# Kernel tuning notes

Hardware: AMD Instinct MI355X
Metric: run time of the kernel (lower is better)

Reference implementation:

```python
import jax, jax.numpy as jnp
import numpy as np

N, NB, NP, T = 1024, 16, 256, 80
EPS_LEN = 1e-9   # seg_len clamp_min in original
EPS_DD = 1e-12   # dot(d,d) clamp_min in original


def setup_inputs() -> dict:
    key = jax.random.key(0)
    k1, k2, k3, k4 = jax.random.split(key, 4)
    # smooth-ish random trajectory (cumsum of steps)
    selected_traj = jnp.cumsum(jax.random.normal(k1, (N, T, 3), jnp.float32) * 0.5, axis=1)
    # random polylines per (sample, boundary)
    road_points = jnp.cumsum(jax.random.normal(k2, (N, NB, NP, 3), jnp.float32) * 0.5, axis=2) \
                  + jax.random.normal(k3, (N, NB, 1, 3), jnp.float32) * 2.0
    # ragged valid-prefix masks, length in [2, NP]
    lengths = jax.random.randint(k4, (N, NB), 2, NP + 1)
    road_mask = jnp.arange(NP)[None, None, :] < lengths[:, :, None]
    return {"selected_traj": selected_traj, "road_points": road_points, "road_mask": road_mask}


def _arc_project(pos, rp, rm):
    # pos: [N,T,3]; rp: [N,NB,NP,3]; rm: [N,NB,NP] bool
    n, t = pos.shape[0], pos.shape[1]
    nb, npts = rp.shape[1], rp.shape[2]
    inf = jnp.asarray(jnp.inf, pos.dtype)
    ar = jnp.arange(npts)
    n_valid = rm.sum(-1)                                    # [N,NB]

    # pack valid points to the front, preserving order (== boolean-mask gather in torch)
    order = jnp.argsort(jnp.logical_not(rm), axis=-1, stable=True)
    pts_f = jnp.take_along_axis(rp, order[..., None], axis=2)      # [N,NB,NP,3]
    pack_mask = ar[None, None, :] < n_valid[:, :, None]
    pts_f = jnp.where(pack_mask[..., None], pts_f, 0.0)
    # flipped direction: reverse the valid prefix
    flip_idx = jnp.clip(n_valid[:, :, None] - 1 - ar[None, None, :], 0, npts - 1)
    pts_b = jnp.take_along_axis(pts_f, flip_idx[..., None], axis=2)
    pts_b = jnp.where(pack_mask[..., None], pts_b, 0.0)
    pts = jnp.stack([pts_f, pts_b], axis=2)                 # [N,NB,2,NP,3]

    # segment i is real iff i < n_valid-1
    seg_mask = ar[: npts - 1][None, None, None, :] < (n_valid - 1)[:, :, None, None]  # [N,NB,1,NP-1]
    seg_vec = pts[..., 1:, :] - pts[..., :-1, :]            # [N,NB,2,NP-1,3]
    seg_norm = jnp.sqrt((seg_vec ** 2).sum(-1))
    seg_len = jnp.where(seg_mask, jnp.maximum(seg_norm, EPS_LEN), 0.0)
    cum_s = jnp.concatenate([jnp.zeros_like(seg_len[..., :1]), jnp.cumsum(seg_len, -1)], -1)  # [N,NB,2,NP]
    last_idx = jnp.clip(n_valid - 1, 0, npts - 1)[:, :, None, None]
    total_s = jnp.take_along_axis(cum_s, jnp.broadcast_to(last_idx, (n, nb, 2, 1)), -1)  # [N,NB,2,1]

    # entry: project first trajectory point onto nearest valid segment
    p0 = pos[:, 0][:, None, None, None, :]                  # [N,1,1,1,3]
    a0 = pts[..., :-1, :]
    dd0 = jnp.maximum((seg_vec ** 2).sum(-1), EPS_DD)
    t0 = jnp.clip(((p0 - a0) * seg_vec).sum(-1) / dd0, 0.0, 1.0)
    q0 = a0 + t0[..., None] * seg_vec
    d2 = jnp.where(seg_mask, ((p0 - q0) ** 2).sum(-1), inf)
    seg0 = jnp.argmin(d2, -1)[..., None]                    # [N,NB,2,1]
    entry_s = jnp.take_along_axis(cum_s, seg0, -1) + jnp.take_along_axis(t0 * seg_len, seg0, -1)

    # trajectory arc-length, resample polyline at entry_s + traj arc length
    traj_seg = jnp.sqrt(((pos[:, 1:] - pos[:, :-1]) ** 2).sum(-1))
    traj_cs = jnp.concatenate([jnp.zeros_like(traj_seg[:, :1]), jnp.cumsum(traj_seg, -1)], -1)  # [N,T]
    target_s = jnp.clip(entry_s + traj_cs[:, None, None, :], 0.0, total_s)  # [N,NB,2,T]

    j = jax.vmap(lambda c, tg: jnp.searchsorted(c, tg, side='right'))(
        cum_s.reshape(-1, npts), target_s.reshape(-1, t)) - 1
    j = jnp.clip(j.reshape(n, nb, 2, t), 0, jnp.maximum(n_valid[:, :, None, None] - 2, 0))

    seg_l = jnp.take_along_axis(seg_len, j, -1)
    cs_j = jnp.take_along_axis(cum_s, j, -1)
    t_loc = jnp.clip((target_s - cs_j) / jnp.maximum(seg_l, EPS_LEN), 0.0, 1.0)
    pa = jnp.take_along_axis(pts, j[..., None], axis=3)
    pb = jnp.take_along_axis(pts, (j + 1)[..., None], axis=3)
    proj = pa + t_loc[..., None] * (pb - pa)                # [N,NB,2,T,3]

    # pick (boundary, direction) candidate with min total L2 cost
    cost = jnp.sqrt(((pos[:, None, None] - proj) ** 2).sum(-1)).sum(-1)  # [N,NB,2]
    cand_ok = (n_valid >= 2)[:, :, None]
    cost = jnp.where(cand_ok, cost, inf)
    best = jnp.argmin(cost.reshape(n, -1), -1)
    best_proj = jnp.take_along_axis(proj.reshape(n, -1, t, 3), best[:, None, None, None], axis=1)[:, 0]
    has = cand_ok.any((1, 2))
    return jnp.where(has[:, None, None], best_proj, pos)


def reference(selected_traj, road_points, road_mask):
    pos = selected_traj[..., 0:3]
    out_pos = _arc_project(pos, road_points, road_mask)
    return jnp.concatenate([out_pos, selected_traj[..., 3:]], axis=-1)
```

## Files before the change

kernel.cpp:

```cpp
#include <hip/hip_runtime.h>
#include <math.h>

#define NN 1024
#define NBB 16
#define NP 256
#define TT 80
#define EPS_LEN 1e-9f
#define EPS_DD 1e-12f

__device__ __forceinline__ float frcp(float x){ return __builtin_amdgcn_rcpf(x); }
__device__ __forceinline__ float fsq(float x){ return __builtin_amdgcn_sqrtf(x); }
__device__ __forceinline__ float rlane_f(float x, int l){
  return __builtin_bit_cast(float, __builtin_amdgcn_readlane(__builtin_bit_cast(int, x), l));
}
__device__ __forceinline__ float bump(float v){
  return __builtin_bit_cast(float, __builtin_bit_cast(int, v) + 1);
}

template<int CTRL,int RM>
__device__ __forceinline__ float dpp_add(float v){
  int t = __builtin_amdgcn_update_dpp(0, __builtin_bit_cast(int, v), CTRL, RM, 0xf, true);
  return v + __builtin_bit_cast(float, t);
}
__device__ __forceinline__ float wave_incl_scan(float v){
  v = dpp_add<0x111,0xf>(v);
  v = dpp_add<0x112,0xf>(v);
  v = dpp_add<0x114,0xf>(v);
  v = dpp_add<0x118,0xf>(v);
  v = dpp_add<0x142,0xa>(v);
  v = dpp_add<0x143,0xc>(v);
  return v;
}
__device__ __forceinline__ float wave_sum(float v){ return rlane_f(wave_incl_scan(v), 63); }
template<int CTRL,int RM>
__device__ __forceinline__ float dpp_min(float v){
  int t = __builtin_amdgcn_update_dpp(0x7f800000, __builtin_bit_cast(int,v), CTRL, RM, 0xf, false);
  return fminf(v, __builtin_bit_cast(float,t));
}
__device__ __forceinline__ float wave_min_all(float v){
  v=dpp_min<0x111,0xf>(v); v=dpp_min<0x112,0xf>(v);
  v=dpp_min<0x114,0xf>(v); v=dpp_min<0x118,0xf>(v);
  v=dpp_min<0x142,0xa>(v); v=dpp_min<0x143,0xc>(v);
  return rlane_f(v, 63);
}

__device__ __forceinline__ void lds_fence() {
  __builtin_amdgcn_wave_barrier();
  asm volatile("s_waitcnt lgkmcnt(0)" ::: "memory");
  __builtin_amdgcn_wave_barrier();
}

__device__ __forceinline__ int wave_nv(const void* mask, size_t base, int lane) {
  bool as_byte = ((const unsigned char*)mask)[1] != 0;
  int nv = 0;
  if (as_byte) {
    uchar4 v = ((const uchar4*)((const unsigned char*)mask + base))[lane];
    nv += __popcll(__ballot(v.x != 0));
    nv += __popcll(__ballot(v.y != 0));
    nv += __popcll(__ballot(v.z != 0));
    nv += __popcll(__ballot(v.w != 0));
  } else {
    int4 v = ((const int4*)((const int*)mask + base))[lane];
    nv += __popcll(__ballot(v.x != 0));
    nv += __popcll(__ballot(v.y != 0));
    nv += __popcll(__ballot(v.z != 0));
    nv += __popcll(__ballot(v.w != 0));
  }
  return nv;
}

__device__ __forceinline__ int count256s(const float* __restrict__ cs,
                                         const float* co, float v){
  int K = 0;
  #pragma unroll
  for (int k=0;k<16;k++) K += (co[k] < v);
  int base = (K < 16 ? K : 15) * 16;
  const float4* f4 = (const float4*)(cs + base);
  float4 c0=f4[0], c1=f4[1], c2=f4[2], c3=f4[3];
  int r = (c0.x<v)+(c0.y<v)+(c0.z<v)+(c0.w<v)+(c1.x<v)+(c1.y<v)+(c1.z<v)+(c1.w<v)
        + (c2.x<v)+(c2.y<v)+(c2.z<v)+(c2.w<v)+(c3.x<v)+(c3.y<v)+(c3.z<v)+(c3.w<v);
  return (K >= 16) ? 256 : (base + r);
}

struct SegOut {
  float cpre[4];
  float run;
  float bdf, btf; int bjf;
  float bdl, btl; int bjl;
};

template<bool NEEDMIN>
__device__ __forceinline__ void seg_pass(float4 A, float4 B, float4 C,
                                         int lane, int nv,
                                         float p0x, float p0y, float p0z,
                                         float* __restrict__ pts, SegOut& R) {
  const int j0 = lane * 4;
  float x[5], y[5], z[5];
  x[0]=A.x; y[0]=A.y; z[0]=A.z;
  x[1]=A.w; y[1]=B.x; z[1]=B.y;
  x[2]=B.z; y[2]=B.w; z[2]=C.x;
  x[3]=C.y; y[3]=C.z; z[3]=C.w;
  x[4]=__shfl_down(x[0],1,64); y[4]=__shfl_down(y[0],1,64); z[4]=__shfl_down(z[0],1,64);
  ((float4*)pts)[lane*3+0] = make_float4(x[0],y[0],z[0],x[1]);
  ((float4*)pts)[lane*3+1] = make_float4(y[1],z[1],x[2],y[2]);
  ((float4*)pts)[lane*3+2] = make_float4(z[2],x[3],y[3],z[3]);
  float run = 0.f;
  R.bdf=INFINITY; R.btf=0.f; R.bjf=j0;
  R.bdl=INFINITY; R.btl=0.f; R.bjl=j0;
  #pragma unroll
  for (int k=0;k<4;k++){
    bool valid = (j0+k) < nv-1;
    float vx=x[k+1]-x[k], vy=y[k+1]-y[k], vz=z[k+1]-z[k];
    float n2 = vx*vx+vy*vy+vz*vz;
    float sl = valid ? fmaxf(fsq(n2), EPS_LEN) : 0.f;
    if (NEEDMIN){
      float t = ((p0x-x[k])*vx+(p0y-y[k])*vy+(p0z-z[k])*vz) * frcp(fmaxf(n2,EPS_DD));
      t = fminf(fmaxf(t,0.f),1.f);
      float qx=x[k]+t*vx, qy=y[k]+t*vy, qz=z[k]+t*vz;
      float dx=p0x-qx, dy=p0y-qy, dz=p0z-qz;
      float d2 = valid ? (dx*dx+dy*dy+dz*dz) : INFINITY;
      if (d2 <  R.bdf){R.bdf=d2; R.bjf=j0+k; R.btf=t;}
      if (d2 <= R.bdl){R.bdl=d2; R.bjl=j0+k; R.btl=t;}
    }
    run += sl; R.cpre[k]=run;
  }
  R.run = run;
}

__device__ __forceinline__ void cs_pair_from_regs(int idx, float ex, const SegOut& R,
                                                  float& c0, float& c1){
  int o = idx >> 2, r = idx & 3;
  float a0 = (r==0)?0.f : (r==1)?R.cpre[0] : (r==2)?R.cpre[1] : R.cpre[2];
  float a1 = (r==0)?R.cpre[0] : (r==1)?R.cpre[1] : (r==2)?R.cpre[2] : R.run;
  c0 = rlane_f(ex + a0, idx >> 2);
  c1 = rlane_f(ex + a1, o);
}

__device__ __forceinline__ void interp_at(const float* __restrict__ pts,
                                          const float* __restrict__ cs,
                                          const float* co, float Tot, int nv, int jmaxv,
                                          int dir, float ts,
                                          float& prx, float& pry, float& prz){
  float vq = dir ? (Tot - ts) : bump(ts);
  int cnt = count256s(cs, co, vq);
  int j = dir ? (nv-1-cnt) : (cnt-1);
  j = j<0?0:(j>jmaxv?jmaxv:j);
  int ia = dir ? (nv-1-j) : j;
  int ib = dir ? (nv-2-j) : (j+1);
  int lo = dir ? ib : ia;
  float c_lo = cs[lo], c_hi = cs[lo+1];
  float base = dir ? (Tot - c_hi) : c_lo;
  float tl = (ts - base) * frcp(fmaxf(c_hi - c_lo, EPS_LEN));
  tl = fminf(fmaxf(tl,0.f),1.f);
  float3 PA = *(const float3*)(pts + ia*3);
  float3 PB = *(const float3*)(pts + ib*3);
  prx = PA.x + tl*(PB.x-PA.x);
  pry = PA.y + tl*(PB.y-PA.y);
  prz = PA.z + tl*(PB.z-PA.z);
}

__device__ __forceinline__ void traj_tcs_wave(const float* __restrict__ pos, int lane,
                                              float* __restrict__ s_tc,
                                              float3& ptl, float3& pB){
  ptl.x = pos[lane*3+0]; ptl.y = pos[lane*3+1]; ptl.z = pos[lane*3+2];
  pB = make_float3(0.f,0.f,0.f);
  if (lane < 16){
    int t = 64+lane;
    pB.x = pos[t*3+0]; pB.y = pos[t*3+1]; pB.z = pos[t*3+2];
  }
  float nx = __shfl_down(ptl.x,1,64), ny = __shfl_down(ptl.y,1,64), nz = __shfl_down(ptl.z,1,64);
  float bx0 = rlane_f(pB.x,0), by0 = rlane_f(pB.y,0), bz0 = rlane_f(pB.z,0);
  if (lane==63){ nx=bx0; ny=by0; nz=bz0; }
  float dx=nx-ptl.x, dy=ny-ptl.y, dz=nz-ptl.z;
  float segA = fsq(dx*dx+dy*dy+dz*dz);
  float mx = __shfl_down(pB.x,1,64), my = __shfl_down(pB.y,1,64), mz = __shfl_down(pB.z,1,64);
  float ex=mx-pB.x, ey=my-pB.y, ez=mz-pB.z;
  float segB = (lane<15) ? fsq(ex*ex+ey*ey+ez*ez) : 0.f;
  float incA = wave_incl_scan(segA);
  float totA = rlane_f(incA, 63);
  float incB = wave_incl_scan(segB);
  s_tc[lane+1] = incA;
  if (lane<15) s_tc[65+lane] = totA + incB;
  if (lane==0) s_tc[0] = 0.f;
}

__global__ __launch_bounds__(256, 8)
void cost_kernel(const float* __restrict__ traj, const float* __restrict__ rp,
                 const void* __restrict__ mask,
                 float* __restrict__ cost, float2* __restrict__ ent) {
  __shared__ float s_pts[4][NP*3], s_cs[4][NP], s_tc[4][TT];
  const int wid = threadIdx.x>>6, lane = threadIdx.x&63;
  const int nb = blockIdx.x*4 + wid;
  const int n = nb >> 4;
  const float* pos = traj + (size_t)n*TT*3;

  const float4* p4 = (const float4*)(rp + (size_t)nb*NP*3);
  float4 A = p4[lane*3+0], B = p4[lane*3+1], C = p4[lane*3+2];
  int nvr = wave_nv(mask, (size_t)nb*NP, lane);
  float3 ptl, pB;
  traj_tcs_wave(pos, lane, s_tc[wid], ptl, pB);

  if (nvr < 2){
    if (lane==0){ cost[nb*2+0]=INFINITY; cost[nb*2+1]=INFINITY; }
    return;
  }
  const int nv = nvr;
  float p0x = rlane_f(ptl.x,0), p0y = rlane_f(ptl.y,0), p0z = rlane_f(ptl.z,0);

  SegOut R;
  seg_pass<true>(A,B,C, lane, nv, p0x,p0y,p0z, s_pts[wid], R);

  float inc = wave_incl_scan(R.run);
  float ex = inc - R.run;
  ((float4*)s_cs[wid])[lane] = make_float4(ex, ex+R.cpre[0], ex+R.cpre[1], ex+R.cpre[2]);
  const float Tot = rlane_f(inc, 63);

  float cval = ex + R.cpre[2];
  float co[16];
  #pragma unroll
  for (int k=0;k<16;k++) co[k] = rlane_f(cval, 4*k+3);

  float minv = wave_min_all(R.bdf);
  unsigned long long mf = __ballot(R.bdf == minv);
  unsigned long long ml = __ballot(R.bdl == minv);
  int lf = __builtin_ctzll(mf);
  int ll = 63 - __builtin_clzll(ml);
  int   jf = __builtin_amdgcn_readlane(R.bjf, lf);
  float tf = rlane_f(R.btf, lf);
  int   jl = __builtin_amdgcn_readlane(R.bjl, ll);
  float tl0 = rlane_f(R.btl, ll);
  float cjf, cjf1, cjl, cjl1;
  cs_pair_from_regs(jf, ex, R, cjf, cjf1);
  cs_pair_from_regs(jl, ex, R, cjl, cjl1);
  float e0 = cjf + tf*(cjf1-cjf);
  float e1 = (Tot - cjl1) + (1.f-tl0)*(cjl1-cjl);

  lds_fence();

  const float* cs = s_cs[wid];
  const float* pts = s_pts[wid];
  const float* tcw = s_tc[wid];
  const int jmaxv = nv-2;
  float accf=0.f, accr=0.f;
  #pragma unroll
  for (int p=0;p<3;p++){
    int task = p*64 + lane;
    bool act = task < 2*TT;
    int dir = task>=TT ? 1 : 0;
    int t = dir ? task-TT : task;
    int tr = t < TT ? t : TT-1;
    float ts = (dir ? e1 : e0) + tcw[tr];
    ts = fminf(fmaxf(ts,0.f),Tot);
    float prx,pry,prz;
    interp_at(pts, cs, co, Tot, nv, jmaxv, dir, ts, prx,pry,prz);
    if (p==0){
      float dx=ptl.x-prx, dy=ptl.y-pry, dz=ptl.z-prz;
      accf += fsq(dx*dx+dy*dy+dz*dz);
    } else if (act){
      float px_, py_, pz_;
      if (p==1 && !dir){ px_=pB.x; py_=pB.y; pz_=pB.z; }
      else { px_=pos[t*3+0]; py_=pos[t*3+1]; pz_=pos[t*3+2]; }
      float dx=px_-prx, dy=py_-pry, dz=pz_-prz;
      float dd=fsq(dx*dx+dy*dy+dz*dz);
      if (dir) accr+=dd; else accf+=dd;
    }
  }
  float cf = wave_sum(accf), cr = wave_sum(accr);
  if (lane==0){
    cost[nb*2+0]=cf; cost[nb*2+1]=cr;
    ent[nb] = make_float2(e0, e1);
  }
}

__global__ __launch_bounds__(256)
void winner_kernel(const float* __restrict__ traj, const float* __restrict__ rp,
                   const void* __restrict__ mask,
                   const float* __restrict__ cost, const float2* __restrict__ ent,
                   float* __restrict__ out) {
  __shared__ float s_pts[4][NP*3], s_cs[4][NP], s_tc[4][TT];
  const int wid = threadIdx.x>>6, lane = threadIdx.x&63;
  const int n = blockIdx.x*4 + wid;
  const float* c = cost + (size_t)n*NBB*2;
  float bc = (lane<NBB*2) ? c[lane] : INFINITY;
  int bi = (lane<NBB*2) ? lane : 64;
  #pragma unroll
  for (int d=1;d<64;d<<=1){
    float oc=__shfl_xor(bc,d,64); int oi=__shfl_xor(bi,d,64);
    if (oc<bc || (oc==bc && oi<bi)){bc=oc;bi=oi;}
  }
  const float* pos = traj + (size_t)n*TT*3;
  float* o = out + (size_t)n*TT*3;
  if (bc == INFINITY){
    if (lane < 60) ((float4*)o)[lane] = ((const float4*)pos)[lane];
    return;
  }
  int b = bi>>1, dir = bi&1;
  const size_t nbi = (size_t)n*NBB + b;
  const float4* p4 = (const float4*)(rp + nbi*NP*3);
  float4 A = p4[lane*3+0], B = p4[lane*3+1], C = p4[lane*3+2];
  float2 eW = ent[nbi];
  float entry = dir ? eW.y : eW.x;
  int nv = wave_nv(mask, nbi*NP, lane);
  nv = max(nv, 2);
  float3 ptl, pB;
  traj_tcs_wave(pos, lane, s_tc[wid], ptl, pB);

  SegOut R;
  seg_pass<false>(A,B,C, lane, nv, 0.f,0.f,0.f, s_pts[wid], R);
  float inc = wave_incl_scan(R.run);
  float ex = inc - R.run;
  ((float4*)s_cs[wid])[lane] = make_float4(ex, ex+R.cpre[0], ex+R.cpre[1], ex+R.cpre[2]);
  const float Tot = rlane_f(inc, 63);
  float cval = ex + R.cpre[2];
  float co[16];
  #pragma unroll
  for (int k=0;k<16;k++) co[k] = rlane_f(cval, 4*k+3);

  lds_fence();

  const float* cs = s_cs[wid];
  const float* pts = s_pts[wid];
  const float* tcw = s_tc[wid];
  const int jmaxv = nv-2;
  #pragma unroll
  for (int p=0;p<2;p++){
    int t = p*64 + lane;
    int tr = t < TT ? t : TT-1;
    float ts = entry + tcw[tr];
    ts = fminf(fmaxf(ts,0.f),Tot);
    float prx,pry,prz;
    interp_at(pts, cs, co, Tot, nv, jmaxv, dir, ts, prx,pry,prz);
    if (t < TT){ o[t*3+0]=prx; o[t*3+1]=pry; o[t*3+2]=prz; }
  }
}

extern "C" void kernel_launch(void* const* d_in, const int* in_sizes, int n_in,
                              void* d_out, int out_size, void* d_ws, size_t ws_size,
                              hipStream_t stream) {
  const float* traj = (const float*)d_in[0];
  const float* rp   = (const float*)d_in[1];
  const void*  mask = d_in[2];
  float* cost = (float*)d_ws;
  float2* ent = (float2*)(cost + (size_t)NN*NBB*2);
  float* out  = (float*)d_out;

  hipLaunchKernelGGL(cost_kernel, dim3(NN*NBB/4), dim3(256), 0, stream,
                     traj, rp, mask, cost, ent);
  hipLaunchKernelGGL(winner_kernel, dim3(NN/4), dim3(256), 0, stream,
                     traj, rp, mask, cost, ent, out);
}
```

Measured before the change: 31.94 us.

## Fuse cost and winner kernels into one per-sample block kernel

Replaces the two-kernel pipeline, which wrote costs to a workspace, with a single kernel that uses one 512-thread block per sample. Each of its 8 waves handles two boundaries in sequence and keeps costs and entry points in shared memory. After a block barrier, two waves compute the winning projection, each covering 40 timesteps. This removes a kernel launch, the global workspace round trip and the repeated trajectory prefix computation. In exchange, each wave does its boundaries serially, the grid has fewer blocks, and most waves sit idle during the final phase.

Measured after the change: 30.92 us. 1.03x faster.

```diff
diff --git a/kernel.cpp b/kernel.cpp
--- a/kernel.cpp
+++ b/kernel.cpp
@@ -132,7 +132,7 @@
   int o = idx >> 2, r = idx & 3;
   float a0 = (r==0)?0.f : (r==1)?R.cpre[0] : (r==2)?R.cpre[1] : R.cpre[2];
   float a1 = (r==0)?R.cpre[0] : (r==1)?R.cpre[1] : (r==2)?R.cpre[2] : R.run;
-  c0 = rlane_f(ex + a0, idx >> 2);
+  c0 = rlane_f(ex + a0, o);
   c1 = rlane_f(ex + a1, o);
 }
 
@@ -184,132 +184,126 @@
   if (lane==0) s_tc[0] = 0.f;
 }
 
-__global__ __launch_bounds__(256, 8)
-void cost_kernel(const float* __restrict__ traj, const float* __restrict__ rp,
-                 const void* __restrict__ mask,
-                 float* __restrict__ cost, float2* __restrict__ ent) {
-  __shared__ float s_pts[4][NP*3], s_cs[4][NP], s_tc[4][TT];
+__global__ __launch_bounds__(512, 8)
+void fused_all(const float* __restrict__ traj, const float* __restrict__ rp,
+               const void* __restrict__ mask, float* __restrict__ out) {
+  __shared__ float s_pts[8][NP*3];
+  __shared__ float s_cs[8][NP];
+  __shared__ float s_tc[8][TT];
+  __shared__ float s_cost[NBB*2];
+  __shared__ float2 s_ent[NBB];
+
   const int wid = threadIdx.x>>6, lane = threadIdx.x&63;
-  const int nb = blockIdx.x*4 + wid;
-  const int n = nb >> 4;
+  const int n = blockIdx.x;
   const float* pos = traj + (size_t)n*TT*3;
 
-  const float4* p4 = (const float4*)(rp + (size_t)nb*NP*3);
-  float4 A = p4[lane*3+0], B = p4[lane*3+1], C = p4[lane*3+2];
-  int nvr = wave_nv(mask, (size_t)nb*NP, lane);
   float3 ptl, pB;
   traj_tcs_wave(pos, lane, s_tc[wid], ptl, pB);
-
-  if (nvr < 2){
-    if (lane==0){ cost[nb*2+0]=INFINITY; cost[nb*2+1]=INFINITY; }
-    return;
-  }
-  const int nv = nvr;
-  float p0x = rlane_f(ptl.x,0), p0y = rlane_f(ptl.y,0), p0z = rlane_f(ptl.z,0);
-
-  SegOut R;
-  seg_pass<true>(A,B,C, lane, nv, p0x,p0y,p0z, s_pts[wid], R);
-
-  float inc = wave_incl_scan(R.run);
-  float ex = inc - R.run;
-  ((float4*)s_cs[wid])[lane] = make_float4(ex, ex+R.cpre[0], ex+R.cpre[1], ex+R.cpre[2]);
-  const float Tot = rlane_f(inc, 63);
-
-  float cval = ex + R.cpre[2];
-  float co[16];
-  #pragma unroll
-  for (int k=0;k<16;k++) co[k] = rlane_f(cval, 4*k+3);
-
-  float minv = wave_min_all(R.bdf);
-  unsigned long long mf = __ballot(R.bdf == minv);
-  unsigned long long ml = __ballot(R.bdl == minv);
-  int lf = __builtin_ctzll(mf);
-  int ll = 63 - __builtin_clzll(ml);
-  int   jf = __builtin_amdgcn_readlane(R.bjf, lf);
-  float tf = rlane_f(R.btf, lf);
-  int   jl = __builtin_amdgcn_readlane(R.bjl, ll);
-  float tl0 = rlane_f(R.btl, ll);
-  float cjf, cjf1, cjl, cjl1;
-  cs_pair_from_regs(jf, ex, R, cjf, cjf1);
-  cs_pair_from_regs(jl, ex, R, cjl, cjl1);
-  float e0 = cjf + tf*(cjf1-cjf);
-  float e1 = (Tot - cjl1) + (1.f-tl0)*(cjl1-cjl);
-
-  lds_fence();
-
-  const float* cs = s_cs[wid];
-  const float* pts = s_pts[wid];
+  const float p0x = rlane_f(ptl.x,0), p0y = rlane_f(ptl.y,0), p0z = rlane_f(ptl.z,0);
+
+  float* pts = s_pts[wid];
+  float* csb = s_cs[wid];
   const float* tcw = s_tc[wid];
-  const int jmaxv = nv-2;
-  float accf=0.f, accr=0.f;
-  #pragma unroll
-  for (int p=0;p<3;p++){
-    int task = p*64 + lane;
-    bool act = task < 2*TT;
-    int dir = task>=TT ? 1 : 0;
-    int t = dir ? task-TT : task;
-    int tr = t < TT ? t : TT-1;
-    float ts = (dir ? e1 : e0) + tcw[tr];
-    ts = fminf(fmaxf(ts,0.f),Tot);
-    float prx,pry,prz;
-    interp_at(pts, cs, co, Tot, nv, jmaxv, dir, ts, prx,pry,prz);
-    if (p==0){
-      float dx=ptl.x-prx, dy=ptl.y-pry, dz=ptl.z-prz;
-      accf += fsq(dx*dx+dy*dy+dz*dz);
-    } else if (act){
-      float px_, py_, pz_;
-      if (p==1 && !dir){ px_=pB.x; py_=pB.y; pz_=pB.z; }
-      else { px_=pos[t*3+0]; py_=pos[t*3+1]; pz_=pos[t*3+2]; }
-      float dx=px_-prx, dy=py_-pry, dz=pz_-prz;
-      float dd=fsq(dx*dx+dy*dy+dz*dz);
-      if (dir) accr+=dd; else accf+=dd;
+
+  #pragma unroll 1
+  for (int c=0; c<2; ++c){
+    const int b = wid*2 + c;
+    const size_t nb = (size_t)n*NBB + b;
+    const float4* p4 = (const float4*)(rp + nb*NP*3);
+    float4 A = p4[lane*3+0], B = p4[lane*3+1], C = p4[lane*3+2];
+    int nv = wave_nv(mask, nb*NP, lane);
+    float cf = INFINITY, cr = INFINITY, e0 = 0.f, e1 = 0.f;
+    if (nv >= 2){
+      SegOut R;
+      seg_pass<true>(A,B,C, lane, nv, p0x,p0y,p0z, pts, R);
+      float inc = wave_incl_scan(R.run);
+      float ex = inc - R.run;
+      ((float4*)csb)[lane] = make_float4(ex, ex+R.cpre[0], ex+R.cpre[1], ex+R.cpre[2]);
+      const float Tot = rlane_f(inc, 63);
+      float cval = ex + R.cpre[2];
+      float co[16];
+      #pragma unroll
+      for (int k=0;k<16;k++) co[k] = rlane_f(cval, 4*k+3);
+      float minv = wave_min_all(R.bdf);
+      unsigned long long mf = __ballot(R.bdf == minv);
+      unsigned long long ml = __ballot(R.bdl == minv);
+      int lf = __builtin_ctzll(mf);
+      int ll = 63 - __builtin_clzll(ml);
+      int   jf = __builtin_amdgcn_readlane(R.bjf, lf);
+      float tf = rlane_f(R.btf, lf);
+      int   jl = __builtin_amdgcn_readlane(R.bjl, ll);
+      float tl0 = rlane_f(R.btl, ll);
+      float cjf, cjf1, cjl, cjl1;
+      cs_pair_from_regs(jf, ex, R, cjf, cjf1);
+      cs_pair_from_regs(jl, ex, R, cjl, cjl1);
+      e0 = cjf + tf*(cjf1-cjf);
+      e1 = (Tot - cjl1) + (1.f-tl0)*(cjl1-cjl);
+
+      lds_fence();
+
+      const int jmaxv = nv-2;
+      float accf=0.f, accr=0.f;
+      #pragma unroll
+      for (int p=0;p<3;p++){
+        int task = p*64 + lane;
+        bool act = task < 2*TT;
+        int dir = task>=TT ? 1 : 0;
+        int t = dir ? task-TT : task;
+        int tr = t < TT ? t : TT-1;
+        float ts = (dir ? e1 : e0) + tcw[tr];
+        ts = fminf(fmaxf(ts,0.f),Tot);
+        float prx,pry,prz;
+        interp_at(pts, csb, co, Tot, nv, jmaxv, dir, ts, prx,pry,prz);
+        if (p==0){
+          float dx=ptl.x-prx, dy=ptl.y-pry, dz=ptl.z-prz;
+          accf += fsq(dx*dx+dy*dy+dz*dz);
+        } else if (act){
+          float px_, py_, pz_;
+          if (p==1 && !dir){ px_=pB.x; py_=pB.y; pz_=pB.z; }
+          else { px_=pos[t*3+0]; py_=pos[t*3+1]; pz_=pos[t*3+2]; }
+          float dx=px_-prx, dy=py_-pry, dz=pz_-prz;
+          float dd=fsq(dx*dx+dy*dy+dz*dz);
+          if (dir) accr+=dd; else accf+=dd;
+        }
+      }
+      cf = wave_sum(accf); cr = wave_sum(accr);
+      lds_fence();
     }
-  }
-  float cf = wave_sum(accf), cr = wave_sum(accr);
-  if (lane==0){
-    cost[nb*2+0]=cf; cost[nb*2+1]=cr;
-    ent[nb] = make_float2(e0, e1);
-  }
-}
-
-__global__ __launch_bounds__(256)
-void winner_kernel(const float* __restrict__ traj, const float* __restrict__ rp,
-                   const void* __restrict__ mask,
-                   const float* __restrict__ cost, const float2* __restrict__ ent,
-                   float* __restrict__ out) {
-  __shared__ float s_pts[4][NP*3], s_cs[4][NP], s_tc[4][TT];
-  const int wid = threadIdx.x>>6, lane = threadIdx.x&63;
-  const int n = blockIdx.x*4 + wid;
-  const float* c = cost + (size_t)n*NBB*2;
-  float bc = (lane<NBB*2) ? c[lane] : INFINITY;
+    if (lane==0){
+      s_cost[b*2+0]=cf; s_cost[b*2+1]=cr;
+      s_ent[b] = make_float2(e0, e1);
+    }
+  }
+
+  __syncthreads();
+  if (wid >= 2) return;
+
+  float bc = (lane<NBB*2) ? s_cost[lane] : INFINITY;
   int bi = (lane<NBB*2) ? lane : 64;
   #pragma unroll
   for (int d=1;d<64;d<<=1){
     float oc=__shfl_xor(bc,d,64); int oi=__shfl_xor(bi,d,64);
     if (oc<bc || (oc==bc && oi<bi)){bc=oc;bi=oi;}
   }
-  const float* pos = traj + (size_t)n*TT*3;
   float* o = out + (size_t)n*TT*3;
   if (bc == INFINITY){
-    if (lane < 60) ((float4*)o)[lane] = ((const float4*)pos)[lane];
+    if (wid==0 && lane < 60) ((float4*)o)[lane] = ((const float4*)pos)[lane];
     return;
   }
   int b = bi>>1, dir = bi&1;
   const size_t nbi = (size_t)n*NBB + b;
   const float4* p4 = (const float4*)(rp + nbi*NP*3);
   float4 A = p4[lane*3+0], B = p4[lane*3+1], C = p4[lane*3+2];
-  float2 eW = ent[nbi];
+  float2 eW = s_ent[b];
   float entry = dir ? eW.y : eW.x;
   int nv = wave_nv(mask, nbi*NP, lane);
   nv = max(nv, 2);
-  float3 ptl, pB;
-  traj_tcs_wave(pos, lane, s_tc[wid], ptl, pB);
 
   SegOut R;
-  seg_pass<false>(A,B,C, lane, nv, 0.f,0.f,0.f, s_pts[wid], R);
+  seg_pass<false>(A,B,C, lane, nv, 0.f,0.f,0.f, pts, R);
   float inc = wave_incl_scan(R.run);
   float ex = inc - R.run;
-  ((float4*)s_cs[wid])[lane] = make_float4(ex, ex+R.cpre[0], ex+R.cpre[1], ex+R.cpre[2]);
+  ((float4*)csb)[lane] = make_float4(ex, ex+R.cpre[0], ex+R.cpre[1], ex+R.cpre[2]);
   const float Tot = rlane_f(inc, 63);
   float cval = ex + R.cpre[2];
   float co[16];
@@ -318,19 +312,14 @@
 
   lds_fence();
 
-  const float* cs = s_cs[wid];
-  const float* pts = s_pts[wid];
-  const float* tcw = s_tc[wid];
   const int jmaxv = nv-2;
-  #pragma unroll
-  for (int p=0;p<2;p++){
-    int t = p*64 + lane;
-    int tr = t < TT ? t : TT-1;
-    float ts = entry + tcw[tr];
+  int t = wid*40 + lane;
+  if (lane < 40){
+    float ts = entry + tcw[t];
     ts = fminf(fmaxf(ts,0.f),Tot);
     float prx,pry,prz;
-    interp_at(pts, cs, co, Tot, nv, jmaxv, dir, ts, prx,pry,prz);
-    if (t < TT){ o[t*3+0]=prx; o[t*3+1]=pry; o[t*3+2]=prz; }
+    interp_at(pts, csb, co, Tot, nv, jmaxv, dir, ts, prx,pry,prz);
+    o[t*3+0]=prx; o[t*3+1]=pry; o[t*3+2]=prz;
   }
 }
 
@@ -340,12 +329,7 @@
   const float* traj = (const float*)d_in[0];
   const float* rp   = (const float*)d_in[1];
   const void*  mask = d_in[2];
-  float* cost = (float*)d_ws;
-  float2* ent = (float2*)(cost + (size_t)NN*NBB*2);
   float* out  = (float*)d_out;
-
-  hipLaunchKernelGGL(cost_kernel, dim3(NN*NBB/4), dim3(256), 0, stream,
-                     traj, rp, mask, cost, ent);
-  hipLaunchKernelGGL(winner_kernel, dim3(NN/4), dim3(256), 0, stream,
-                     traj, rp, mask, cost, ent, out);
-}
+  hipLaunchKernelGGL(fused_all, dim3(NN), dim3(512), 0, stream,
+                     traj, rp, mask, out);
+}
```
